# Optimization experiments

Measured on AMD Instinct MI355X. Metric: run time of the kernel, lower is better.

The kernel has to match this reference:

```python
import jax, jax.numpy as jnp
import numpy as np

T, D_IN, D_OUT, E = 4096, 1024, 4096, 8


def setup_inputs() -> dict:
    key = jax.random.key(0)
    k1, k2, k3 = jax.random.split(key, 3)
    input_tensor = jax.random.normal(k1, (T, D_IN), dtype=jnp.float32)
    # tokens are pre-sorted by expert; contiguous counts per expert (sum == T)
    expert_token_cnt = jnp.full((E,), T // E, dtype=jnp.int32)
    # learned params: nn.init.normal_(mean=0, std=1)
    weight = jax.random.normal(k2, (E, D_OUT, D_IN), dtype=jnp.float32)
    bias = jax.random.normal(k3, (E, D_OUT), dtype=jnp.float32)
    return {"input_tensor": input_tensor, "expert_token_cnt": expert_token_cnt,
            "weight": weight, "bias": bias}


def reference(input_tensor, expert_token_cnt, weight, bias):
    # Grouped GEMM: token t in segment e computes y[t] = x[t] @ W[e].T + b[e]
    # followed by exact (erf) GELU. dropout_rate = 0.0 -> identity.
    n_tok = input_tensor.shape[0]
    n_exp = weight.shape[0]
    bounds = jnp.cumsum(expert_token_cnt)                       # [E]
    expert_id = jnp.searchsorted(bounds, jnp.arange(n_tok), side='right')  # [T]
    onehot = (expert_id[:, None] == jnp.arange(n_exp)[None, :]).astype(input_tensor.dtype)  # [T,E]
    y = jnp.zeros((n_tok, weight.shape[1]), dtype=input_tensor.dtype)
    for e in range(n_exp):  # fixed small expert count; each iter is one masked GEMM
        xe = input_tensor * onehot[:, e][:, None]               # zero out other experts' tokens
        y = y + jnp.einsum('ti,oi->to', xe, weight[e])
    y = y + bias[expert_id]                                     # per-token expert bias
    y = jax.nn.gelu(y, approximate=False)                       # torch default exact GELU
    return y
```

## Files before the change

kernel.cpp:

```cpp
#include <hip/hip_runtime.h>
#include <hip/hip_bf16.h>
#include <math.h>

#define T_TOK 4096
#define DIN   1024
#define DOUT  4096
#define NEXP  8

#define BM 256
#define BN 256
#define BK 64
#define NT (DIN / BK)

typedef __bf16 bf16x8 __attribute__((ext_vector_type(8)));
typedef float  f32x4  __attribute__((ext_vector_type(4)));
typedef unsigned short u16x8 __attribute__((ext_vector_type(8)));

__device__ __forceinline__ unsigned short f2bf(float f) {
    union { float f; unsigned u; } x; x.f = f;
    unsigned r = x.u + 0x7FFFu + ((x.u >> 16) & 1u);
    return (unsigned short)(r >> 16);
}

__global__ __launch_bounds__(256) void convert_all(
        const float* __restrict__ srcA, unsigned short* __restrict__ dstA,
        const float* __restrict__ srcW, unsigned short* __restrict__ dstW) {
    const int nA = T_TOK * DIN / 8;
    const int nW = NEXP * DOUT * DIN / 8;
    int i = blockIdx.x * blockDim.x + threadIdx.x;
    const int stride = gridDim.x * blockDim.x;
    for (; i < nA + nW; i += stride) {
        const float* s; unsigned short* d; int idx;
        if (i < nA) { s = srcA; d = dstA; idx = i; }
        else        { s = srcW; d = dstW; idx = i - nA; }
        const f32x4* p = (const f32x4*)(s + (size_t)idx * 8);
        f32x4 v0 = p[0], v1 = p[1];
        u16x8 o;
        #pragma unroll
        for (int q = 0; q < 4; ++q) { o[q] = f2bf(v0[q]); o[4 + q] = f2bf(v1[q]); }
        *(u16x8*)(d + (size_t)idx * 8) = o;
    }
}

__device__ __forceinline__ void gload_lds16(const __bf16* g, __bf16* l) {
    __builtin_amdgcn_global_load_lds(
        (const __attribute__((address_space(1))) unsigned int*)g,
        (__attribute__((address_space(3))) unsigned int*)l,
        16, 0, 0);
}

__global__ __launch_bounds__(512, 2) void moe_gemm(
        const __bf16* __restrict__ A, const __bf16* __restrict__ W,
        const float* __restrict__ bias, const int* __restrict__ cnt,
        float* __restrict__ C) {
    __shared__ __bf16 Asm[2][BM * BK];
    __shared__ __bf16 Bsm[2][BN * BK];

    const int tid  = threadIdx.x;
    const int wid  = tid >> 6;
    const int lane = tid & 63;

    int bid = blockIdx.x;
    bid = (bid & 7) * 32 + (bid >> 3);
    const int mt = bid >> 4;
    const int nt = bid & 15;
    const int m0 = mt * BM;
    const int n0 = nt * BN;

    int e = 0, csum = 0;
    #pragma unroll
    for (int i = 0; i < NEXP; ++i) {
        int c = cnt[i];
        if (m0 >= csum + c) { csum += c; e = i + 1; }
    }

    const __bf16* Ab = A + (size_t)m0 * DIN;
    const __bf16* Wb = W + (size_t)e * DOUT * DIN + (size_t)n0 * DIN;

    const int srow = lane >> 3;
    const int sgx  = (lane & 7) ^ srow;

    const int wr_ = wid >> 2;
    const int wc_ = wid & 3;
    const int fr  = lane & 15;
    const int fh  = lane >> 4;

    f32x4 acc[8][4];
    #pragma unroll
    for (int i = 0; i < 8; ++i)
        #pragma unroll
        for (int j = 0; j < 4; ++j)
            acc[i][j] = (f32x4)(0.0f);

    auto stage = [&](int b, int kt) {
        #pragma unroll
        for (int s = 0; s < 4; ++s) {
            const int rbase = wid * 32 + s * 8;
            gload_lds16(Ab + (size_t)(rbase + srow) * DIN + kt + sgx * 8,
                        &Asm[b][rbase * BK]);
        }
        #pragma unroll
        for (int s = 0; s < 4; ++s) {
            const int rbase = wid * 32 + s * 8;
            gload_lds16(Wb + (size_t)(rbase + srow) * DIN + kt + sgx * 8,
                        &Bsm[b][rbase * BK]);
        }
    };

    auto compute = [&](int b) {
        #pragma unroll
        for (int ks = 0; ks < 2; ++ks) {
            bf16x8 af[8], bf[4];
            #pragma unroll
            for (int i = 0; i < 8; ++i) {
                const int r = wr_ * 128 + i * 16 + fr;
                const int g = (ks * 4 + fh) ^ (r & 7);
                af[i] = *(const bf16x8*)&Asm[b][r * BK + g * 8];
            }
            #pragma unroll
            for (int j = 0; j < 4; ++j) {
                const int r = wc_ * 64 + j * 16 + fr;
                const int g = (ks * 4 + fh) ^ (r & 7);
                bf[j] = *(const bf16x8*)&Bsm[b][r * BK + g * 8];
            }
            #pragma unroll
            for (int i = 0; i < 8; ++i)
                #pragma unroll
                for (int j = 0; j < 4; ++j)
                    acc[i][j] = __builtin_amdgcn_mfma_f32_16x16x32_bf16(
                                    af[i], bf[j], acc[i][j], 0, 0, 0);
        }
    };

    stage(0, 0);
    __syncthreads();
    int cur = 0;
    for (int t = 0; t < NT - 1; ++t) {
        stage(cur ^ 1, (t + 1) * BK);
        compute(cur);
        __syncthreads();
        cur ^= 1;
    }
    compute(cur);

    const int colf = lane & 15;
    const int rowf = fh * 4;
    #pragma unroll
    for (int j = 0; j < 4; ++j) {
        const int col = n0 + wc_ * 64 + j * 16 + colf;
        const float bv = bias[(size_t)e * DOUT + col];
        #pragma unroll
        for (int i = 0; i < 8; ++i) {
            #pragma unroll
            for (int r = 0; r < 4; ++r) {
                const int row = m0 + wr_ * 128 + i * 16 + rowf + r;
                float x = acc[i][j][r] + bv;
                float g = 0.5f * x * (1.0f + erff(x * 0.70710678118654752f));
                C[(size_t)row * DOUT + col] = g;
            }
        }
    }
}

extern "C" void kernel_launch(void* const* d_in, const int* in_sizes, int n_in,
                              void* d_out, int out_size, void* d_ws, size_t ws_size,
                              hipStream_t stream) {
    (void)in_sizes; (void)n_in; (void)out_size; (void)ws_size;
    const float* input  = (const float*)d_in[0];
    const int*   cnt    = (const int*)d_in[1];
    const float* weight = (const float*)d_in[2];
    const float* bias   = (const float*)d_in[3];
    float* out = (float*)d_out;

    unsigned short* a_bf = (unsigned short*)d_ws;
    unsigned short* w_bf = a_bf + (size_t)T_TOK * DIN;

    hipLaunchKernelGGL(convert_all, dim3(2048), dim3(256), 0, stream,
                       input, a_bf, weight, w_bf);

    dim3 grid((T_TOK / BM) * (DOUT / BN));
    hipLaunchKernelGGL(moe_gemm, grid, dim3(512), 0, stream,
                       (const __bf16*)a_bf, (const __bf16*)w_bf, bias, cnt, out);
}
```

Before: 292.1 us.

## Stream fp32 weights directly into LDS and convert in GEMM, triple-buffer pipeline

Drops the separate weight fp32-to-bf16 conversion pass, which read 128MB and wrote 64MB. The GEMM now loads fp32 weights straight into LDS and converts them to bf16 in registers before the MFMAs. To fit LDS, BK is halved to 32, and the double buffer becomes a triple buffer with explicit vmcnt waits and s_setprio. The cost is that each block reads fp32 weights, which doubles weight traffic inside the GEMM, and the conversion ALU work is repeated across the 16 M-tiles that share each weight tile.

New measurement: 273.5 us. 6.4% less time.

```diff
diff --git a/kernel.cpp b/kernel.cpp
--- a/kernel.cpp
+++ b/kernel.cpp
@@ -9,7 +9,7 @@
 
 #define BM 256
 #define BN 256
-#define BK 64
+#define BK 32
 #define NT (DIN / BK)
 
 typedef __bf16 bf16x8 __attribute__((ext_vector_type(8)));
@@ -22,27 +22,22 @@
     return (unsigned short)(r >> 16);
 }
 
-__global__ __launch_bounds__(256) void convert_all(
-        const float* __restrict__ srcA, unsigned short* __restrict__ dstA,
-        const float* __restrict__ srcW, unsigned short* __restrict__ dstW) {
-    const int nA = T_TOK * DIN / 8;
-    const int nW = NEXP * DOUT * DIN / 8;
+__global__ __launch_bounds__(256) void convert_A(
+        const float* __restrict__ src, unsigned short* __restrict__ dst) {
+    const int n = T_TOK * DIN / 8;
     int i = blockIdx.x * blockDim.x + threadIdx.x;
     const int stride = gridDim.x * blockDim.x;
-    for (; i < nA + nW; i += stride) {
-        const float* s; unsigned short* d; int idx;
-        if (i < nA) { s = srcA; d = dstA; idx = i; }
-        else        { s = srcW; d = dstW; idx = i - nA; }
-        const f32x4* p = (const f32x4*)(s + (size_t)idx * 8);
+    for (; i < n; i += stride) {
+        const f32x4* p = (const f32x4*)(src + (size_t)i * 8);
         f32x4 v0 = p[0], v1 = p[1];
         u16x8 o;
         #pragma unroll
         for (int q = 0; q < 4; ++q) { o[q] = f2bf(v0[q]); o[4 + q] = f2bf(v1[q]); }
-        *(u16x8*)(d + (size_t)idx * 8) = o;
-    }
-}
-
-__device__ __forceinline__ void gload_lds16(const __bf16* g, __bf16* l) {
+        *(u16x8*)(dst + (size_t)i * 8) = o;
+    }
+}
+
+__device__ __forceinline__ void gload_lds16(const void* g, void* l) {
     __builtin_amdgcn_global_load_lds(
         (const __attribute__((address_space(1))) unsigned int*)g,
         (__attribute__((address_space(3))) unsigned int*)l,
@@ -50,11 +45,11 @@
 }
 
 __global__ __launch_bounds__(512, 2) void moe_gemm(
-        const __bf16* __restrict__ A, const __bf16* __restrict__ W,
+        const __bf16* __restrict__ A, const float* __restrict__ W,
         const float* __restrict__ bias, const int* __restrict__ cnt,
         float* __restrict__ C) {
-    __shared__ __bf16 Asm[2][BM * BK];
-    __shared__ __bf16 Bsm[2][BN * BK];
+    __shared__ __bf16 Asm[3][BM * BK];
+    __shared__ float  Bsm[3][BN * BK];
 
     const int tid  = threadIdx.x;
     const int wid  = tid >> 6;
@@ -75,15 +70,19 @@
     }
 
     const __bf16* Ab = A + (size_t)m0 * DIN;
-    const __bf16* Wb = W + (size_t)e * DOUT * DIN + (size_t)n0 * DIN;
-
-    const int srow = lane >> 3;
-    const int sgx  = (lane & 7) ^ srow;
+    const float*  Wb = W + (size_t)e * DOUT * DIN + (size_t)n0 * DIN;
+
+    const int sArow = lane >> 2;
+    const int sgA   = (lane & 3) ^ ((lane >> 3) & 3);
+    const int sBrow = lane >> 3;
+    const int sgB   = (lane & 7) ^ sBrow;
 
     const int wr_ = wid >> 2;
     const int wc_ = wid & 3;
     const int fr  = lane & 15;
     const int fh  = lane >> 4;
+    const int gA  = fh ^ ((fr >> 1) & 3);
+    const int gB0 = (2 * fh) ^ (fr & 7);
 
     f32x4 acc[8][4];
     #pragma unroll
@@ -94,54 +93,78 @@
 
     auto stage = [&](int b, int kt) {
         #pragma unroll
+        for (int s = 0; s < 2; ++s) {
+            const int rb = wid * 32 + s * 16;
+            gload_lds16(Ab + (size_t)(rb + sArow) * DIN + kt + sgA * 8,
+                        &Asm[b][rb * BK]);
+        }
+        #pragma unroll
         for (int s = 0; s < 4; ++s) {
-            const int rbase = wid * 32 + s * 8;
-            gload_lds16(Ab + (size_t)(rbase + srow) * DIN + kt + sgx * 8,
-                        &Asm[b][rbase * BK]);
-        }
-        #pragma unroll
-        for (int s = 0; s < 4; ++s) {
-            const int rbase = wid * 32 + s * 8;
-            gload_lds16(Wb + (size_t)(rbase + srow) * DIN + kt + sgx * 8,
-                        &Bsm[b][rbase * BK]);
+            const int rb = wid * 32 + s * 8;
+            gload_lds16(Wb + (size_t)(rb + sBrow) * DIN + kt + sgB * 4,
+                        &Bsm[b][rb * BK]);
         }
     };
 
     auto compute = [&](int b) {
-        #pragma unroll
-        for (int ks = 0; ks < 2; ++ks) {
-            bf16x8 af[8], bf[4];
+        bf16x8 af[8];
+        #pragma unroll
+        for (int i = 0; i < 8; ++i) {
+            const int r = wr_ * 128 + i * 16 + fr;
+            af[i] = *(const bf16x8*)&Asm[b][r * BK + gA * 8];
+        }
+        __builtin_amdgcn_s_setprio(1);
+        #pragma unroll
+        for (int j = 0; j < 4; ++j) {
+            const int c = wc_ * 64 + j * 16 + fr;
+            f32x4 lo = *(const f32x4*)&Bsm[b][c * BK + gB0 * 4];
+            f32x4 hi = *(const f32x4*)&Bsm[b][c * BK + (gB0 ^ 1) * 4];
+            bf16x8 bv;
             #pragma unroll
-            for (int i = 0; i < 8; ++i) {
-                const int r = wr_ * 128 + i * 16 + fr;
-                const int g = (ks * 4 + fh) ^ (r & 7);
-                af[i] = *(const bf16x8*)&Asm[b][r * BK + g * 8];
-            }
-            #pragma unroll
-            for (int j = 0; j < 4; ++j) {
-                const int r = wc_ * 64 + j * 16 + fr;
-                const int g = (ks * 4 + fh) ^ (r & 7);
-                bf[j] = *(const bf16x8*)&Bsm[b][r * BK + g * 8];
+            for (int q = 0; q < 4; ++q) {
+                bv[q]     = (__bf16)lo[q];
+                bv[4 + q] = (__bf16)hi[q];
             }
             #pragma unroll
             for (int i = 0; i < 8; ++i)
-                #pragma unroll
-                for (int j = 0; j < 4; ++j)
-                    acc[i][j] = __builtin_amdgcn_mfma_f32_16x16x32_bf16(
-                                    af[i], bf[j], acc[i][j], 0, 0, 0);
-        }
+                acc[i][j] = __builtin_amdgcn_mfma_f32_16x16x32_bf16(
+                                af[i], bv, acc[i][j], 0, 0, 0);
+        }
+        __builtin_amdgcn_s_setprio(0);
     };
 
     stage(0, 0);
-    __syncthreads();
-    int cur = 0;
-    for (int t = 0; t < NT - 1; ++t) {
-        stage(cur ^ 1, (t + 1) * BK);
-        compute(cur);
-        __syncthreads();
-        cur ^= 1;
-    }
-    compute(cur);
+    stage(1, BK);
+    asm volatile("s_waitcnt vmcnt(6)" ::: "memory");
+    __builtin_amdgcn_s_barrier();
+    __builtin_amdgcn_sched_barrier(0);
+
+    #pragma unroll 1
+    for (int s = 0; s < (NT - 2) / 3; ++s) {
+        const int t = 3 * s;
+        stage(2, (t + 2) * BK);
+        compute(0);
+        asm volatile("s_waitcnt vmcnt(6)" ::: "memory");
+        __builtin_amdgcn_s_barrier();
+        __builtin_amdgcn_sched_barrier(0);
+
+        stage(0, (t + 3) * BK);
+        compute(1);
+        asm volatile("s_waitcnt vmcnt(6)" ::: "memory");
+        __builtin_amdgcn_s_barrier();
+        __builtin_amdgcn_sched_barrier(0);
+
+        stage(1, (t + 4) * BK);
+        compute(2);
+        asm volatile("s_waitcnt vmcnt(6)" ::: "memory");
+        __builtin_amdgcn_s_barrier();
+        __builtin_amdgcn_sched_barrier(0);
+    }
+    compute(0);
+    asm volatile("s_waitcnt vmcnt(0)" ::: "memory");
+    __builtin_amdgcn_s_barrier();
+    __builtin_amdgcn_sched_barrier(0);
+    compute(1);
 
     const int colf = lane & 15;
     const int rowf = fh * 4;
@@ -173,12 +196,11 @@
     float* out = (float*)d_out;
 
     unsigned short* a_bf = (unsigned short*)d_ws;
-    unsigned short* w_bf = a_bf + (size_t)T_TOK * DIN;
-
-    hipLaunchKernelGGL(convert_all, dim3(2048), dim3(256), 0, stream,
-                       input, a_bf, weight, w_bf);
+
+    hipLaunchKernelGGL(convert_A, dim3(1024), dim3(256), 0, stream,
+                       input, a_bf);
 
     dim3 grid((T_TOK / BM) * (DOUT / BN));
     hipLaunchKernelGGL(moe_gemm, grid, dim3(512), 0, stream,
-                       (const __bf16*)a_bf, (const __bf16*)w_bf, bias, cnt, out);
-}
+                       (const __bf16*)a_bf, weight, bias, cnt, out);
+}
```

## Deepen GEMM pipeline to four LDS stages with BK=32 and vmcnt waits

Applied to the files above, without the earlier changes.

Replaces the double-buffered BK=64 K-loop with a four-buffer BK=32 pipeline that keeps three tile loads in flight. Each step waits with explicit s_waitcnt vmcnt plus a barrier instead of a full __syncthreads drain. The LDS swizzle is redone for 32-wide rows, and MFMA blocks are wrapped in s_setprio. The intent is to hide global-to-LDS latency better, at the cost of more barriers per K and a fragile hand-counted vmcnt schedule.

Result: no change. 294.1 us (+0.7%).

```diff
diff --git a/kernel.cpp b/kernel.cpp
--- a/kernel.cpp
+++ b/kernel.cpp
@@ -9,8 +9,8 @@
 
 #define BM 256
 #define BN 256
-#define BK 64
-#define NT (DIN / BK)
+#define BK2 32
+#define NU (DIN / BK2)
 
 typedef __bf16 bf16x8 __attribute__((ext_vector_type(8)));
 typedef float  f32x4  __attribute__((ext_vector_type(4)));
@@ -42,19 +42,25 @@
     }
 }
 
-__device__ __forceinline__ void gload_lds16(const __bf16* g, __bf16* l) {
+__device__ __forceinline__ void gload_lds16(const void* g, void* l) {
     __builtin_amdgcn_global_load_lds(
         (const __attribute__((address_space(1))) unsigned int*)g,
         (__attribute__((address_space(3))) unsigned int*)l,
         16, 0, 0);
 }
 
+#define WAITB(N) do {                                             \
+    asm volatile("s_waitcnt vmcnt(" #N ")" ::: "memory");         \
+    __builtin_amdgcn_s_barrier();                                 \
+    asm volatile("" ::: "memory");                                \
+} while (0)
+
 __global__ __launch_bounds__(512, 2) void moe_gemm(
         const __bf16* __restrict__ A, const __bf16* __restrict__ W,
         const float* __restrict__ bias, const int* __restrict__ cnt,
         float* __restrict__ C) {
-    __shared__ __bf16 Asm[2][BM * BK];
-    __shared__ __bf16 Bsm[2][BN * BK];
+    __shared__ __bf16 Asm[4][BM * BK2];
+    __shared__ __bf16 Bsm[4][BN * BK2];
 
     const int tid  = threadIdx.x;
     const int wid  = tid >> 6;
@@ -77,13 +83,14 @@
     const __bf16* Ab = A + (size_t)m0 * DIN;
     const __bf16* Wb = W + (size_t)e * DOUT * DIN + (size_t)n0 * DIN;
 
-    const int srow = lane >> 3;
-    const int sgx  = (lane & 7) ^ srow;
+    const int srow = lane >> 2;
+    const int sgK  = (lane & 3) ^ ((lane >> 3) & 3);
 
     const int wr_ = wid >> 2;
     const int wc_ = wid & 3;
     const int fr  = lane & 15;
     const int fh  = lane >> 4;
+    const int gK  = fh ^ ((fr >> 1) & 3);
 
     f32x4 acc[8][4];
     #pragma unroll
@@ -92,56 +99,61 @@
         for (int j = 0; j < 4; ++j)
             acc[i][j] = (f32x4)(0.0f);
 
-    auto stage = [&](int b, int kt) {
+    auto stage = [&](int b, int u) {
+        const int kt = u * BK2;
         #pragma unroll
-        for (int s = 0; s < 4; ++s) {
-            const int rbase = wid * 32 + s * 8;
-            gload_lds16(Ab + (size_t)(rbase + srow) * DIN + kt + sgx * 8,
-                        &Asm[b][rbase * BK]);
+        for (int s = 0; s < 2; ++s) {
+            const int rb = s * 128 + wid * 16;
+            gload_lds16(Ab + (size_t)(rb + srow) * DIN + kt + sgK * 8,
+                        &Asm[b][rb * BK2]);
         }
         #pragma unroll
-        for (int s = 0; s < 4; ++s) {
-            const int rbase = wid * 32 + s * 8;
-            gload_lds16(Wb + (size_t)(rbase + srow) * DIN + kt + sgx * 8,
-                        &Bsm[b][rbase * BK]);
+        for (int s = 0; s < 2; ++s) {
+            const int rb = s * 128 + wid * 16;
+            gload_lds16(Wb + (size_t)(rb + srow) * DIN + kt + sgK * 8,
+                        &Bsm[b][rb * BK2]);
         }
     };
 
     auto compute = [&](int b) {
+        bf16x8 af[8], bf[4];
         #pragma unroll
-        for (int ks = 0; ks < 2; ++ks) {
-            bf16x8 af[8], bf[4];
+        for (int i = 0; i < 8; ++i) {
+            const int r = wr_ * 128 + i * 16 + fr;
+            af[i] = *(const bf16x8*)&Asm[b][r * BK2 + gK * 8];
+        }
+        #pragma unroll
+        for (int j = 0; j < 4; ++j) {
+            const int c = wc_ * 64 + j * 16 + fr;
+            bf[j] = *(const bf16x8*)&Bsm[b][c * BK2 + gK * 8];
+        }
+        __builtin_amdgcn_s_setprio(1);
+        #pragma unroll
+        for (int i = 0; i < 8; ++i)
             #pragma unroll
-            for (int i = 0; i < 8; ++i) {
-                const int r = wr_ * 128 + i * 16 + fr;
-                const int g = (ks * 4 + fh) ^ (r & 7);
-                af[i] = *(const bf16x8*)&Asm[b][r * BK + g * 8];
-            }
-            #pragma unroll
-            for (int j = 0; j < 4; ++j) {
-                const int r = wc_ * 64 + j * 16 + fr;
-                const int g = (ks * 4 + fh) ^ (r & 7);
-                bf[j] = *(const bf16x8*)&Bsm[b][r * BK + g * 8];
-            }
-            #pragma unroll
-            for (int i = 0; i < 8; ++i)
-                #pragma unroll
-                for (int j = 0; j < 4; ++j)
-                    acc[i][j] = __builtin_amdgcn_mfma_f32_16x16x32_bf16(
-                                    af[i], bf[j], acc[i][j], 0, 0, 0);
-        }
+            for (int j = 0; j < 4; ++j)
+                acc[i][j] = __builtin_amdgcn_mfma_f32_16x16x32_bf16(
+                                af[i], bf[j], acc[i][j], 0, 0, 0);
+        __builtin_amdgcn_s_setprio(0);
     };
 
     stage(0, 0);
-    __syncthreads();
-    int cur = 0;
-    for (int t = 0; t < NT - 1; ++t) {
-        stage(cur ^ 1, (t + 1) * BK);
-        compute(cur);
-        __syncthreads();
-        cur ^= 1;
+    stage(1, 1);
+    stage(2, 2);
+    WAITB(8);
+
+    #pragma unroll 1
+    for (int s = 0; s < 7; ++s) {
+        const int p = 4 * s;
+        stage(3, p + 3); compute(0); WAITB(8);
+        stage(0, p + 4); compute(1); WAITB(8);
+        stage(1, p + 5); compute(2); WAITB(8);
+        stage(2, p + 6); compute(3); WAITB(8);
     }
-    compute(cur);
+    stage(3, 31); compute(0); WAITB(8);
+    compute(1); WAITB(4);
+    compute(2); WAITB(0);
+    compute(3);
 
     const int colf = lane & 15;
     const int rowf = fh * 4;
```
